# Kernel optimization log

Measured on AMD Instinct MI355X. Metric: run time of the kernel, lower is better.

## Reference

```python
import jax, jax.numpy as jnp
import numpy as np

K = 3        # kernel_size
EPS = 1e-4   # eps from __init__


def _conv_valid(x, w):
    # NHWC input, HWIO filter, VALID padding, stride 1
    return jax.lax.conv_general_dilated(
        x, w, window_strides=(1, 1), padding='VALID',
        dimension_numbers=('NHWC', 'HWIO', 'NHWC'))


def _backward_standardize_weight(grad_in, original_weights, gain, w_max_bitmap, eps):
    # Faithful translation of BackwardInjectWSConv2D.backward_standardize_weight
    kh, kw, cin, cout = original_weights.shape
    N = float(kh * kw * cin)                       # b*h*w in the TF code
    mu = jnp.mean(original_weights, axis=(0, 1, 2))
    xmu = original_weights - mu                    # [K,K,Cin,Cout]
    var = jnp.mean(jnp.square(xmu), axis=(0, 1, 2))
    mvar = N * var
    maxvar = jnp.maximum(mvar, eps)
    sqrtvar = jnp.sqrt(maxvar)
    ivar = 1.0 / sqrtvar
    givar = gain * ivar                            # [Cout]
    dgivar = jnp.sum(grad_in * xmu, axis=(0, 1, 2))
    divar = dgivar * gain
    dgain = dgivar * ivar
    dxmu1 = grad_in * givar
    dsqrtvar = (-1.0 / jnp.square(sqrtvar)) * divar
    dmaxvar = (0.5 / jnp.sqrt(maxvar)) * dsqrtvar
    dmvar = w_max_bitmap * dmaxvar
    dvar = N * dmvar
    dsq = (1.0 / N) * dvar                         # (1/N)*ones_like(grad_in)*dvar, broadcast
    dxmu2 = 2.0 * xmu * dsq
    dx1 = dxmu1 + dxmu2
    dmu = -jnp.sum(dx1, axis=(0, 1, 2))
    dx2 = (1.0 / N) * dmu                          # broadcast over [K,K,Cin]
    dx = dx1 + dx2
    return dx, dgain


def setup_inputs() -> dict:
    key = jax.random.key(0)
    ks = jax.random.split(key, 5)
    B, H, W, Cin, Cout = 64, 56, 56, 128, 128
    return {
        'grad_output': jax.random.normal(ks[0], (B, H, W, Cout), jnp.float32),
        'inputs': jax.random.normal(ks[1], (B, H, W, Cin), jnp.float32),
        'kernels': jax.random.normal(ks[2], (K, K, Cin, Cout), jnp.float32),
        'std_kernels': jax.random.normal(ks[3], (K, K, Cin, Cout), jnp.float32),
        'gain': jax.random.uniform(ks[4], (Cout,), jnp.float32),
        'w_max_bitmap': jnp.ones((Cout,), jnp.float32),
    }


def reference(grad_output, inputs, kernels, std_kernels, gain, w_max_bitmap):
    pad = (K - 1) // 2
    # ---- grad wrt input: full conv of grad_out with rot180(std_kernels), io swapped
    go_pad = jnp.pad(grad_output, ((0, 0), (pad, pad), (pad, pad), (0, 0)))
    w_rot = jnp.transpose(std_kernels[::-1, ::-1], (0, 1, 3, 2))   # [K,K,Cout,Cin]
    manual_grad_in = _conv_valid(go_pad, w_rot)                    # [B,H,W,Cin]
    # ---- grad wrt weight: treat Cin as batch, B as contraction channel
    in_pad = jnp.pad(inputs, ((0, 0), (pad, pad), (pad, pad), (0, 0)))
    fmt_inp = jnp.transpose(in_pad, (3, 1, 2, 0))                  # [Cin,H+2p,W+2p,B]
    fmt_wt = jnp.transpose(grad_output, (1, 2, 0, 3))              # [H,W,B,Cout]
    direct = _conv_valid(fmt_inp, fmt_wt)                          # [Cin,K,K,Cout]
    grad_wt_raw = jnp.transpose(direct, (1, 2, 0, 3))              # [K,K,Cin,Cout]
    # ---- weight-standardization backward chain
    manual_grad_wt, manual_grad_gain = _backward_standardize_weight(
        grad_wt_raw, kernels, gain, w_max_bitmap, EPS)
    # ---- bias grad
    manual_grad_bias = jnp.sum(grad_output, axis=(0, 1, 2))        # [Cout]
    return manual_grad_in, manual_grad_wt, manual_grad_bias, manual_grad_gain
```

## Files before the change

### kernel.cpp

```cpp
#include <hip/hip_runtime.h>
#include <hip/hip_bf16.h>

typedef __bf16 bf16x8 __attribute__((ext_vector_type(8)));
typedef __bf16 bf16x4 __attribute__((ext_vector_type(4)));
typedef float  f32x4  __attribute__((ext_vector_type(4)));
typedef unsigned int u32;

#define HW_   3136
#define NPIX  200704
#define GI_ELEMS 25690112

#define GOT_OFF   0u
#define RAW_OFF   51380224u
#define BIASA_OFF 51970048u
#define STDKF_OFF 51970560u
#define GUARD_OFF 52265472u
#define ZB_OFF    52265728u
#define ZA_OFF    52272000u
#define X_OFF     52279168u

__device__ __forceinline__ f32x4 mfma16(bf16x8 a, bf16x8 b, f32x4 c){
  return __builtin_amdgcn_mfma_f32_16x16x32_bf16(a, b, c, 0, 0, 0);
}

__device__ __forceinline__ void async16(const void* g, __bf16* l){
  __builtin_amdgcn_global_load_lds(
      (const __attribute__((address_space(1))) void*)g,
      (__attribute__((address_space(3))) void*)l, 16, 0, 0);
}

__global__ __launch_bounds__(256) void k_prep(const float* __restrict__ s, __bf16* __restrict__ d){
  const int g = blockIdx.x*256 + threadIdx.x;
  const int l = g & 63;
  const int j = (g >> 6) & 7;
  const int kc = (g >> 9) & 3;
  const int tap = g >> 11;
  const int ci = j*16 + (l & 15);
  const int co0 = kc*32 + (l >> 4)*8;
  const float* src = s + ((size_t)(tap*128 + ci))*128 + co0;
  f32x4 x0 = *(const f32x4*)src;
  f32x4 x1 = *(const f32x4*)(src + 4);
  bf16x8 y;
  #pragma unroll
  for (int e=0;e<4;e++){ y[e] = (__bf16)x0[e]; y[e+4] = (__bf16)x1[e]; }
  *(bf16x8*)(d + (size_t)g*8) = y;
}

__global__ __launch_bounds__(256) void k_goT(const float* __restrict__ go,
                                             __bf16* __restrict__ goT,
                                             __bf16* __restrict__ goB,
                                             float* __restrict__ biasA){
  __shared__ __bf16 T[64][130];
  __shared__ float biasS[128];
  const int t = threadIdx.x;
  const size_t p0 = (size_t)blockIdx.x*64;
  if (t < 128) biasS[t] = 0.f;
  __syncthreads();
  float bs[4] = {0.f,0.f,0.f,0.f};
  const int co0 = (t*4) & 127;
  #pragma unroll
  for (int i=0;i<8;i++){
    const int flat = (i*256+t)*4;
    const int px = flat >> 7, co = flat & 127;
    f32x4 x = *(const f32x4*)(go + p0*128 + flat);
    bf16x4 y;
    #pragma unroll
    for (int e=0;e<4;e++){ y[e] = (__bf16)x[e]; bs[e] += x[e]; }
    *(bf16x4*)&T[px][co] = y;
    *(bf16x4*)(goB + p0*128 + flat) = y;
  }
  #pragma unroll
  for (int e=0;e<4;e++) atomicAdd(&biasS[co0+e], bs[e]);
  __syncthreads();
  #pragma unroll
  for (int j=0;j<2;j++){
    const int task = j*256 + t;
    const int co = task >> 2, q = task & 3;
    bf16x8 v0, v1;
    #pragma unroll
    for (int k=0;k<8;k++) v0[k] = T[q*16+k][co];
    #pragma unroll
    for (int k=0;k<8;k++) v1[k] = T[q*16+8+k][co];
    __bf16* d = goT + (size_t)co*NPIX + p0 + q*16;
    *(bf16x8*)d = v0; *(bf16x8*)(d+8) = v1;
  }
  if (t < 128) atomicAdd(&biasA[t], biasS[t]);
}

__global__ __launch_bounds__(256) void k_inT(const float* __restrict__ inp,
                                             __bf16* __restrict__ inT){
  __shared__ __bf16 T[64][130];
  const int t = threadIdx.x;
  const size_t p0 = (size_t)blockIdx.x*64;
  #pragma unroll
  for (int i=0;i<8;i++){
    const int flat = (i*256+t)*4;
    const int px = flat >> 7, ci = flat & 127;
    f32x4 x = *(const f32x4*)(inp + p0*128 + flat);
    bf16x4 y;
    #pragma unroll
    for (int e=0;e<4;e++) y[e] = (__bf16)x[e];
    *(bf16x4*)&T[px][ci] = y;
  }
  __syncthreads();
  #pragma unroll
  for (int j=0;j<4;j++){
    const int task = j*256 + t;
    const int ci = task >> 3, ch = task & 7;
    const int p = (int)p0 + ch*8;
    const int b = p / HW_; const int r = p - b*HW_;
    const int h = r / 56;  const int w = r - h*56;
    bf16x8 v;
    #pragma unroll
    for (int k=0;k<8;k++) v[k] = T[ch*8+k][ci];
    *(bf16x8*)(inT + (((size_t)(ci*64+b))*58 + (h+1))*64 + w) = v;
  }
}

__global__ __launch_bounds__(256) void k_padz(__bf16* __restrict__ inT){
  const int g = blockIdx.x*256 + threadIdx.x;
  const int pair = g / 72, k = g - pair*72;
  __bf16* base = inT + (size_t)pair*3712;
  int off;
  if (k < 8)       off = k*8;
  else if (k < 16) off = 57*64 + (k-8)*8;
  else             off = (k-15)*64 + 56;
  bf16x8 z = {};
  *(bf16x8*)(base + off) = z;
}

__global__ __launch_bounds__(512, 2) void k_gradin4(const __bf16* __restrict__ goB,
                                                    const __bf16* __restrict__ stdkF,
                                                    const __bf16* __restrict__ zsrc,
                                                    float* __restrict__ out){
  __shared__ char LDS[148480];
  const int t = threadIdx.x;
  const int wv = t >> 6, l = t & 63, lr = l & 15, lg = l >> 4;
  const int b = blockIdx.x, h0 = blockIdx.y*8;
  const int j0 = (wv & 1)*4;
  const int pxg = (wv >> 1)*112;

  #pragma unroll
  for (int it=0; it<19; ++it){
    const int qb = it*512 + wv*64;
    if (qb < 9280){
      const u32 q = qb + l;
      const u32 r = q / 928u;
      const u32 rem = q - r*928u;
      const u32 wp = rem >> 4;
      const u32 c = rem & 15u;
      const int h = h0 - 1 + (int)r;
      const u32 s = r*58u + wp;
      const u32 csrc = c ^ (s & 7u);
      const bool valid = (h >= 0) & (h < 56) & (wp >= 1u) & (wp <= 56u);
      const __bf16* src = valid
        ? goB + ((size_t)((b*HW_) + h*56 + ((int)wp - 1))*128 + csrc*8)
        : zsrc;
      async16(src, (__bf16*)(LDS + qb*16));
    }
  }

  int sb[7];
  #pragma unroll
  for (int tile=0; tile<7; ++tile){
    const int p = pxg + tile*16 + lr;
    const int ro = p / 56; const int w = p - ro*56;
    sb[tile] = (ro + 2)*58 + (w + 2);
  }

  f32x4 acc[7][4];
  #pragma unroll
  for (int i=0;i<7;i++){
    #pragma unroll
    for (int j=0;j<4;j++){
      #pragma unroll
      for (int r=0;r<4;r++) acc[i][j][r] = 0.f;
    }
  }
  __syncthreads();

  for (int tap=0; tap<9; ++tap){
    const int u = tap/3;
    const int soff = u*58 + (tap - u*3);
    #pragma unroll
    for (int kc=0; kc<4; ++kc){
      bf16x8 Bf[4];
      #pragma unroll
      for (int j=0;j<4;++j)
        Bf[j] = *(const bf16x8*)(stdkF + ((size_t)(((tap*4 + kc)*8 + j0 + j)*64 + l))*8);
      bf16x8 Af[7];
      #pragma unroll
      for (int tile=0;tile<7;++tile){
        const int s = sb[tile] - soff;
        const int byte = (s << 8) | (((kc*4 + lg) ^ (s & 7)) << 4);
        Af[tile] = *(const bf16x8*)(LDS + byte);
      }
      #pragma unroll
      for (int tile=0;tile<7;++tile){
        #pragma unroll
        for (int j=0;j<4;++j)
          acc[tile][j] = mfma16(Af[tile], Bf[j], acc[tile][j]);
      }
    }
  }

  float* o = out + ((size_t)b*HW_ + (size_t)h0*56 + pxg)*128;
  #pragma unroll
  for (int tile=0;tile<7;++tile){
    #pragma unroll
    for (int j=0;j<4;++j){
      #pragma unroll
      for (int r=0;r<4;++r)
        o[(size_t)(tile*16 + 4*lg + r)*128 + (j0 + j)*16 + lr] = acc[tile][j][r];
    }
  }
}

#define GW_G 29696
#define GW_A 29728

#define KSTEP(ks)                                                              \
{                                                                              \
  const int pl = (ks)*32 + lg*8;                                               \
  const int q  = (ks)*4 + lg;                                                  \
  const int hl = q / 7;                                                        \
  const int w0 = pl - hl*56;                                                   \
  bf16x8 b0 = *(const bf16x8*)&LDS[(wco + lr)*232 + pl];                       \
  bf16x8 b1 = *(const bf16x8*)&LDS[(wco + 16 + lr)*232 + pl];                  \
  const __bf16* abase = &LDS[GW_A + lr*392 + hl*64 + w0];                      \
  _Pragma("unroll")                                                            \
  for (int u=0; u<3; ++u){                                                     \
    const __bf16* ap = abase + u*64;                                           \
    union { bf16x8 v; u32 d[4]; } vp, va, vn, a0, a2;                          \
    vp.v = *(const bf16x8*)(ap - 8);                                           \
    va.v = *(const bf16x8*)ap;                                                 \
    vn.v = *(const bf16x8*)(ap + 8);                                           \
    a0.d[0] = (va.d[0] << 16) | (vp.d[3] >> 16);                               \
    a0.d[1] = (va.d[1] << 16) | (va.d[0] >> 16);                               \
    a0.d[2] = (va.d[2] << 16) | (va.d[1] >> 16);                               \
    a0.d[3] = (va.d[3] << 16) | (va.d[2] >> 16);                               \
    a2.d[0] = (va.d[0] >> 16) | (va.d[1] << 16);                               \
    a2.d[1] = (va.d[1] >> 16) | (va.d[2] << 16);                               \
    a2.d[2] = (va.d[2] >> 16) | (va.d[3] << 16);                               \
    a2.d[3] = (va.d[3] >> 16) | (vn.d[0] << 16);                               \
    acc[u*3+0][0] = mfma16(a0.v, b0, acc[u*3+0][0]);                           \
    acc[u*3+0][1] = mfma16(a0.v, b1, acc[u*3+0][1]);                           \
    acc[u*3+1][0] = mfma16(va.v, b0, acc[u*3+1][0]);                           \
    acc[u*3+1][1] = mfma16(va.v, b1, acc[u*3+1][1]);                           \
    acc[u*3+2][0] = mfma16(a2.v, b0, acc[u*3+2][0]);                           \
    acc[u*3+2][1] = mfma16(a2.v, b1, acc[u*3+2][1]);                           \
  }                                                                            \
}

__global__ __launch_bounds__(256, 2) void k_gradwt7(const char* __restrict__ ws,
                                                    float* __restrict__ raw){
  __shared__ __bf16 LDS[36000];
  const int t = threadIdx.x;
  const int w = t >> 6, l = t & 63, lr = l & 15, lg = l >> 4;
  const int b = blockIdx.x, ci0 = blockIdx.y*16;
  const int wco = w*32;

  if (t < 32) LDS[GW_G + t] = (__bf16)0.f;

  u32 boff[15];
  #pragma unroll
  for (int i=0;i<15;i++){
    const int chunk = i*256 + w*64 + l;
    if (chunk < 3712){
      const int co = chunk / 29, part = chunk - co*29;
      boff[i] = (part < 28)
        ? (GOT_OFF + (u32)(co*NPIX + b*HW_ + part*8)*2u)
        : ZB_OFF;
    } else boff[i] = ZB_OFF;
  }
  u32 aoff[4];
  #pragma unroll
  for (int i=0;i<4;i++){
    const int chunk = i*256 + w*64 + l;
    if (chunk < 784){
      const int ci = chunk / 49, r = chunk - ci*49;
      aoff[i] = (r < 48)
        ? (X_OFF + (u32)((((ci0+ci)*64 + b)*58 + (r>>3))*64 + (r&7)*8)*2u)
        : ZA_OFF;
    } else aoff[i] = ZA_OFF;
  }

  f32x4 acc[9][2];
  #pragma unroll
  for (int tp=0;tp<9;tp++){
    #pragma unroll
    for (int j=0;j<2;j++){
      #pragma unroll
      for (int r=0;r<4;r++) acc[tp][j][r] = 0.f;
    }
  }

  for (int c=0; c<14; ++c){
    #pragma unroll
    for (int i=0;i<15;i++){
      if (i < 14 || w < 2){
        async16(ws + boff[i], LDS + (i*256 + w*64)*8);
        boff[i] += 448u;
      }
    }
    #pragma unroll
    for (int i=0;i<4;i++){
      const int chunk = i*256 + w*64 + l;
      if (chunk < 784){
        async16(ws + aoff[i], LDS + GW_A + (i*256 + w*64)*8);
        aoff[i] += 512u;
      }
    }
    __syncthreads();

    KSTEP(0) KSTEP(1) KSTEP(2) KSTEP(3) KSTEP(4) KSTEP(5) KSTEP(6)

    __syncthreads();
  }

  #pragma unroll
  for (int tp=0;tp<9;tp++){
    #pragma unroll
    for (int j=0;j<2;j++){
      #pragma unroll
      for (int r=0;r<4;r++)
        atomicAdd(&raw[(size_t)(tp*128 + ci0 + 4*lg + r)*128 + wco + j*16 + lr],
                  acc[tp][j][r]);
    }
  }
}

__global__ __launch_bounds__(128) void k_std(const float* __restrict__ raw,
      const float* __restrict__ kern, const float* __restrict__ gain,
      const float* __restrict__ bmap, const float* __restrict__ biasA,
      float* __restrict__ out_wt, float* __restrict__ out_bias, float* __restrict__ out_gain){
  const int co = blockIdx.x, t = threadIdx.x;
  float kv[9], gv[9];
  float s1=0.f, s2=0.f, sg=0.f, sgk=0.f;
  #pragma unroll
  for (int i=0;i<9;i++){
    const int m = t + i*128;
    const float k_ = kern[(size_t)m*128 + co];
    const float g_ = raw [(size_t)m*128 + co];
    kv[i]=k_; gv[i]=g_;
    s1 += k_; s2 += k_*k_; sg += g_; sgk += g_*k_;
  }
  __shared__ float red[4][128];
  red[0][t]=s1; red[1][t]=s2; red[2][t]=sg; red[3][t]=sgk;
  __syncthreads();
  for (int off=64; off>0; off>>=1){
    if (t < off){
      red[0][t]+=red[0][t+off]; red[1][t]+=red[1][t+off];
      red[2][t]+=red[2][t+off]; red[3][t]+=red[3][t+off];
    }
    __syncthreads();
  }
  const float N = 1152.f;
  const float S1=red[0][0], S2=red[1][0], Sg=red[2][0], Sgk=red[3][0];
  const float mu = S1/N;
  const float var = S2/N - mu*mu;
  const float mvar = N*var;
  const float maxvar = fmaxf(mvar, 1e-4f);
  const float sqrtvar = sqrtf(maxvar);
  const float ivar = 1.f/sqrtvar;
  const float g = gain[co];
  const float givar = g*ivar;
  const float dgivar = Sgk - mu*Sg;
  const float divar = dgivar*g;
  const float dsqrtvar = -divar/maxvar;
  const float dmaxvar = 0.5f*dsqrtvar/sqrtvar;
  const float dsq = bmap[co]*dmaxvar;
  const float dmu = -(givar*Sg + 2.f*dsq*(S1 - N*mu));
  const float dmuN = dmu*(1.f/N);
  #pragma unroll
  for (int i=0;i<9;i++){
    const int m = t + i*128;
    out_wt[(size_t)m*128 + co] = gv[i]*givar + 2.f*(kv[i]-mu)*dsq + dmuN;
  }
  if (t == 0){ out_gain[co] = dgivar*ivar; out_bias[co] = biasA[co]; }
}

extern "C" void kernel_launch(void* const* d_in, const int* in_sizes, int n_in,
                              void* d_out, int out_size, void* d_ws, size_t ws_size,
                              hipStream_t stream){
  const float* go   = (const float*)d_in[0];
  const float* inp  = (const float*)d_in[1];
  const float* kern = (const float*)d_in[2];
  const float* stdk = (const float*)d_in[3];
  const float* gain = (const float*)d_in[4];
  const float* bmap = (const float*)d_in[5];

  char* ws = (char*)d_ws;
  __bf16* goT   = (__bf16*)(ws + GOT_OFF);
  float*  raw   = (float*) (ws + RAW_OFF);
  float*  biasA = (float*) (ws + BIASA_OFF);
  __bf16* stdkF = (__bf16*)(ws + STDKF_OFF);
  char*   guard =           ws + GUARD_OFF;
  __bf16* goB   = (__bf16*)(ws + X_OFF);
  __bf16* inT   = (__bf16*)(ws + X_OFF);

  hipMemsetAsync(ws + RAW_OFF,   0, 589824 + 512, stream);
  hipMemsetAsync(ws + GUARD_OFF, 0, 256 + 6272 + 7168, stream);

  k_prep  <<<72, 256, 0, stream>>>(stdk, stdkF);
  k_goT   <<<3136, 256, 0, stream>>>(go, goT, goB, biasA);
  k_gradin4<<<dim3(64,7), 512, 0, stream>>>(goB, stdkF, (const __bf16*)guard, (float*)d_out);

  k_padz  <<<2304, 256, 0, stream>>>(inT);
  k_inT   <<<3136, 256, 0, stream>>>(inp, inT);
  k_gradwt7<<<dim3(64,8), 256, 0, stream>>>((const char*)ws, raw);

  float* out = (float*)d_out;
  k_std<<<128, 128, 0, stream>>>(raw, kern, gain, bmap, biasA,
                                 out + GI_ELEMS,
                                 out + GI_ELEMS + 147456,
                                 out + GI_ELEMS + 147456 + 128);
}
```

Measured before the change: 300.8 us.

## Split grad-weight kernel over output-channel halves and K-steps across waves

The grad-weight kernel now launches a third grid dimension that splits the 128 output channels into two halves of 64, which halves the grad_output tile staged in LDS per block. Within a block, the four waves are split two ways: by output-channel half and by which subset of the seven K-steps they compute. Pairs of waves therefore accumulate partial sums that are combined through the existing atomics. The smaller LDS footprint lets the launch bounds request three blocks per CU instead of two, with twice as many blocks overall, to raise occupancy. The cost is that the input tile is loaded twice as often, there are twice as many atomic adds, and the K-step split between waves is uneven (four steps versus three).

```diff
diff --git a/kernel.cpp b/kernel.cpp
--- a/kernel.cpp
+++ b/kernel.cpp
@@ -216,8 +216,8 @@
   }
 }
 
-#define GW_G 29696
-#define GW_A 29728
+#define GW_G 14848
+#define GW_A 14880
 
 #define KSTEP(ks)                                                              \
 {                                                                              \
@@ -252,31 +252,33 @@
   }                                                                            \
 }
 
-__global__ __launch_bounds__(256, 2) void k_gradwt7(const char* __restrict__ ws,
+__global__ __launch_bounds__(256, 3) void k_gradwt8(const char* __restrict__ ws,
                                                     float* __restrict__ raw){
-  __shared__ __bf16 LDS[36000];
+  __shared__ __bf16 LDS[21152];
   const int t = threadIdx.x;
-  const int w = t >> 6, l = t & 63, lr = l & 15, lg = l >> 4;
+  const int wv = t >> 6, l = t & 63, lr = l & 15, lg = l >> 4;
   const int b = blockIdx.x, ci0 = blockIdx.y*16;
-  const int wco = w*32;
+  const int co0 = blockIdx.z*64;
+  const int wco = (wv & 1)*32;
+  const int kh = wv >> 1;
 
   if (t < 32) LDS[GW_G + t] = (__bf16)0.f;
 
-  u32 boff[15];
-  #pragma unroll
-  for (int i=0;i<15;i++){
-    const int chunk = i*256 + w*64 + l;
-    if (chunk < 3712){
+  u32 boff[8];
+  #pragma unroll
+  for (int i=0;i<8;i++){
+    const int chunk = i*256 + t;
+    if (chunk < 1856){
       const int co = chunk / 29, part = chunk - co*29;
       boff[i] = (part < 28)
-        ? (GOT_OFF + (u32)(co*NPIX + b*HW_ + part*8)*2u)
+        ? (GOT_OFF + (u32)((co0+co)*NPIX + b*HW_ + part*8)*2u)
         : ZB_OFF;
     } else boff[i] = ZB_OFF;
   }
   u32 aoff[4];
   #pragma unroll
   for (int i=0;i<4;i++){
-    const int chunk = i*256 + w*64 + l;
+    const int chunk = i*256 + t;
     if (chunk < 784){
       const int ci = chunk / 49, r = chunk - ci*49;
       aoff[i] = (r < 48)
@@ -297,23 +299,25 @@
 
   for (int c=0; c<14; ++c){
     #pragma unroll
-    for (int i=0;i<15;i++){
-      if (i < 14 || w < 2){
-        async16(ws + boff[i], LDS + (i*256 + w*64)*8);
+    for (int i=0;i<8;i++){
+      const int chunk = i*256 + t;
+      if (chunk < 1856){
+        async16(ws + boff[i], LDS + (i*256 + (t & ~63))*8 + (t & 63)*8);
         boff[i] += 448u;
       }
     }
     #pragma unroll
     for (int i=0;i<4;i++){
-      const int chunk = i*256 + w*64 + l;
+      const int chunk = i*256 + t;
       if (chunk < 784){
-        async16(ws + aoff[i], LDS + GW_A + (i*256 + w*64)*8);
+        async16(ws + aoff[i], LDS + GW_A + (i*256 + (t & ~63))*8 + (t & 63)*8);
         aoff[i] += 512u;
       }
     }
     __syncthreads();
 
-    KSTEP(0) KSTEP(1) KSTEP(2) KSTEP(3) KSTEP(4) KSTEP(5) KSTEP(6)
+    if (kh == 0){ KSTEP(0) KSTEP(1) KSTEP(2) KSTEP(3) }
+    else        { KSTEP(4) KSTEP(5) KSTEP(6) }
 
     __syncthreads();
   }
@@ -324,7 +328,7 @@
     for (int j=0;j<2;j++){
       #pragma unroll
       for (int r=0;r<4;r++)
-        atomicAdd(&raw[(size_t)(tp*128 + ci0 + 4*lg + r)*128 + wco + j*16 + lr],
+        atomicAdd(&raw[(size_t)(tp*128 + ci0 + 4*lg + r)*128 + co0 + wco + j*16 + lr],
                   acc[tp][j][r]);
     }
   }
@@ -408,7 +412,7 @@
 
   k_padz  <<<2304, 256, 0, stream>>>(inT);
   k_inT   <<<3136, 256, 0, stream>>>(inp, inT);
-  k_gradwt7<<<dim3(64,8), 256, 0, stream>>>((const char*)ws, raw);
+  k_gradwt8<<<dim3(64,8,2), 256, 0, stream>>>((const char*)ws, raw);
 
   float* out = (float*)d_out;
   k_std<<<128, 128, 0, stream>>>(raw, kern, gain, bmap, biasA,
```

New measurement: 373.0 us. 1.24x slower.
